# Kernel optimization log

Measured on AMD Instinct MI355X. Metric: run time of the kernel, lower is better.

The kernel has to match this reference:

```python
import jax, jax.numpy as jnp
import numpy as np

B, T, D = 4, 2048, 1024
H = 16
HD = D // H


def setup_inputs() -> dict:
    key = jax.random.key(0)
    ks = jax.random.split(key, 9)
    s = 1.0 / np.sqrt(D)
    return {
        "x": jax.random.normal(ks[0], (B, T, D), dtype=jnp.float32),
        "Wk": jax.random.normal(ks[1], (D, D), dtype=jnp.float32) * s,
        "bk": jnp.zeros((D,), dtype=jnp.float32),
        "Wq": jax.random.normal(ks[2], (D, D), dtype=jnp.float32) * s,
        "bq": jnp.zeros((D,), dtype=jnp.float32),
        "Wv": jax.random.normal(ks[3], (D, D), dtype=jnp.float32) * s,
        "bv": jnp.zeros((D,), dtype=jnp.float32),
        "Wp": jax.random.normal(ks[4], (D, D), dtype=jnp.float32) * s,
        "bp": jnp.zeros((D,), dtype=jnp.float32),
    }


def reference(x, Wk, bk, Wq, bq, Wv, bv, Wp, bp):
    Bv, Tv, Dv = x.shape
    # project and split heads: [B, H, T, HD]
    def heads(w, b):
        return (x @ w + b).reshape(Bv, Tv, H, HD).transpose(0, 2, 1, 3)
    k = heads(Wk, bk)
    q = heads(Wq, bq)
    v = heads(Wv, bv)
    scale = 1.0 / np.sqrt(HD)
    att = jnp.einsum('bhqd,bhkd->bhqk', q, k) * scale  # [B,H,T,T]
    causal = jnp.tril(jnp.ones((Tv, Tv), dtype=bool))
    att = jnp.where(causal[None, None, :, :], att, -jnp.inf)
    att = jax.nn.softmax(att, axis=-1)
    y = jnp.einsum('bhqk,bhkd->bhqd', att, v)  # [B,H,T,HD]
    y = y.transpose(0, 2, 1, 3).reshape(Bv, Tv, Dv)
    return y @ Wp + bp
```

## Files before the change

### kernel.cpp

```cpp
#include <hip/hip_runtime.h>
#include <stdint.h>

#define Bb 4
#define Tt 2048
#define Dd 1024
#define Hh 16
#define HDd 64
#define Mm 8192

typedef __attribute__((ext_vector_type(8))) short bf16x8;
typedef __attribute__((ext_vector_type(4))) float f32x4;
typedef __attribute__((ext_vector_type(16))) float f32x16;

#define MFMA(a, b, c) __builtin_amdgcn_mfma_f32_16x16x32_bf16(a, b, c, 0, 0, 0)
#define MFMA32(a, b, c) __builtin_amdgcn_mfma_f32_32x32x16_bf16(a, b, c, 0, 0, 0)

#define LOG2E 1.44269504088896340736f
#if __has_builtin(__builtin_amdgcn_exp2f)
#define EXP2(x) __builtin_amdgcn_exp2f(x)
#else
#define EXP2(x) __expf((x) * 0.69314718055994530942f)
#endif

union vfu { uint2 u2[2]; bf16x8 v; };
union apu { uint32_t u[4]; bf16x8 v; };

__device__ __forceinline__ unsigned short f2b(float f) {
  union { float f; uint32_t u; } v; v.f = f;
  return (unsigned short)((v.u + 0x7FFFu + ((v.u >> 16) & 1u)) >> 16);
}

__device__ __forceinline__ uint32_t pk2(float a, float b) {
  union { __bf16 h[2]; uint32_t u; } x;
  x.h[0] = (__bf16)a; x.h[1] = (__bf16)b;
  return x.u;
}

__device__ __forceinline__ void gload_lds16(const void* g, void* l) {
  __builtin_amdgcn_global_load_lds(
      (const __attribute__((address_space(1))) void*)g,
      (__attribute__((address_space(3))) void*)l, 16, 0, 0);
}

__global__ __launch_bounds__(256) void k_convert_x(const float* __restrict__ x,
                                                   unsigned short* __restrict__ xb) {
  int i = (blockIdx.x * 256 + threadIdx.x) * 8;
  float4 a = *(const float4*)(x + i);
  float4 b = *(const float4*)(x + i + 4);
  uint4 o;
  o.x = f2b(a.x) | ((uint32_t)f2b(a.y) << 16);
  o.y = f2b(a.z) | ((uint32_t)f2b(a.w) << 16);
  o.z = f2b(b.x) | ((uint32_t)f2b(b.y) << 16);
  o.w = f2b(b.z) | ((uint32_t)f2b(b.w) << 16);
  *(uint4*)(xb + i) = o;
}

__global__ __launch_bounds__(256) void k_transpose_w(
    const float* __restrict__ Wk, const float* __restrict__ Wq,
    const float* __restrict__ Wv, const float* __restrict__ Wp,
    unsigned short* __restrict__ WkT, unsigned short* __restrict__ WqT,
    unsigned short* __restrict__ WvT, unsigned short* __restrict__ WpT) {
  const float* W; unsigned short* O;
  int wsel = blockIdx.y;
  W = wsel == 0 ? Wk : wsel == 1 ? Wq : wsel == 2 ? Wv : Wp;
  O = wsel == 0 ? WkT : wsel == 1 ? WqT : wsel == 2 ? WvT : WpT;
  __shared__ unsigned short tile[32][36];
  int kb = (blockIdx.x >> 5) << 5;
  int nb = (blockIdx.x & 31) << 5;
  int t = threadIdx.x;
  int r = t >> 3, c4 = (t & 7) << 2;
  float4 v = *(const float4*)(W + (size_t)(kb + r) * Dd + nb + c4);
  tile[r][c4 + 0] = f2b(v.x); tile[r][c4 + 1] = f2b(v.y);
  tile[r][c4 + 2] = f2b(v.z); tile[r][c4 + 3] = f2b(v.w);
  __syncthreads();
  uint2 o;
  o.x = tile[c4 + 0][r] | ((uint32_t)tile[c4 + 1][r] << 16);
  o.y = tile[c4 + 2][r] | ((uint32_t)tile[c4 + 3][r] << 16);
  *(uint2*)(O + (size_t)(nb + r) * Dd + kb + c4) = o;
}

__global__ __launch_bounds__(256, 2) void k_gemm3(
    const unsigned short* __restrict__ A,
    const unsigned short* __restrict__ BtQ, const unsigned short* __restrict__ BtK,
    const unsigned short* __restrict__ BtV,
    const float* __restrict__ bq, const float* __restrict__ bk,
    const float* __restrict__ bv,
    unsigned short* __restrict__ Qb, unsigned short* __restrict__ Kb,
    unsigned short* __restrict__ VTb) {
  __shared__ __align__(16) unsigned short Al[2][128 * 32];
  __shared__ __align__(16) unsigned short Bl[2][3][128 * 32];
  int tid = threadIdx.x;
  int lane = tid & 63, wid = tid >> 6;
  int wr = wid >> 1, wc = wid & 1;
  int lq = lane & 15, lh = lane >> 4;
  int mb = blockIdx.x * 128;
  int nb = blockIdx.y << 7;

  int srow = (wid << 5) + (lane >> 2);
  int scol = (lane & 3) << 3;
  const unsigned short* Ag = A + (size_t)(mb + srow) * Dd + scol;
  const unsigned short* Bg0 = BtQ + (size_t)(nb + srow) * Dd + scol;
  const unsigned short* Bg1 = BtK + (size_t)(nb + srow) * Dd + scol;
  const unsigned short* Bg2 = BtV + (size_t)(nb + srow) * Dd + scol;
  int lofs = wid << 10;

#define STAGE3(kb_, bi_) do {                                            \
    gload_lds16(Ag + (kb_), &Al[bi_][0] + lofs);                         \
    gload_lds16(Ag + (kb_) + 16 * Dd, &Al[bi_][0] + lofs + 16 * 32);     \
    gload_lds16(Bg0 + (kb_), &Bl[bi_][0][0] + lofs);                     \
    gload_lds16(Bg0 + (kb_) + 16 * Dd, &Bl[bi_][0][0] + lofs + 16 * 32); \
    gload_lds16(Bg1 + (kb_), &Bl[bi_][1][0] + lofs);                     \
    gload_lds16(Bg1 + (kb_) + 16 * Dd, &Bl[bi_][1][0] + lofs + 16 * 32); \
    gload_lds16(Bg2 + (kb_), &Bl[bi_][2][0] + lofs);                     \
    gload_lds16(Bg2 + (kb_) + 16 * Dd, &Bl[bi_][2][0] + lofs + 16 * 32); \
  } while (0)

  f32x4 zero = {0.f, 0.f, 0.f, 0.f};
  f32x4 acc[3][4][4];
#pragma unroll
  for (int s = 0; s < 3; s++)
#pragma unroll
    for (int m = 0; m < 4; m++)
#pragma unroll
      for (int n = 0; n < 4; n++) acc[s][m][n] = zero;

  STAGE3(0, 0);
  __syncthreads();

  int cur = 0;
  for (int kb = 0; kb < Dd; kb += 32) {
    if (kb + 32 < Dd) STAGE3(kb + 32, cur ^ 1);
    bf16x8 af[4];
#pragma unroll
    for (int m = 0; m < 4; m++)
      af[m] = *(const bf16x8*)(&Al[cur][0] +
                               (((wr << 6) + (m << 4) + lq) << 5) + (lh << 3));
#pragma unroll
    for (int s = 0; s < 3; s++) {
      bf16x8 bf[4];
#pragma unroll
      for (int n = 0; n < 4; n++)
        bf[n] = *(const bf16x8*)(&Bl[cur][s][0] +
                                 (((wc << 6) + (n << 4) + lq) << 5) + (lh << 3));
      __builtin_amdgcn_s_setprio(1);
#pragma unroll
      for (int m = 0; m < 4; m++)
#pragma unroll
        for (int n = 0; n < 4; n++) acc[s][m][n] = MFMA(af[m], bf[n], acc[s][m][n]);
      __builtin_amdgcn_s_setprio(0);
    }
    __syncthreads();
    cur ^= 1;
  }
#undef STAGE3

  int b_idx = mb >> 11;
#pragma unroll
  for (int s = 0; s < 3; s++) {
#pragma unroll
    for (int n = 0; n < 4; n++) {
      int col = nb + (wc << 6) + (n << 4) + lq;
      float bbias = (s == 0) ? bq[col] : (s == 1) ? bk[col] : bv[col];
      int hh = col >> 6, hd = col & 63;
#pragma unroll
      for (int m = 0; m < 4; m++) {
        int row0 = mb + (wr << 6) + (m << 4) + (lh << 2);
        int t0 = row0 & 2047;
        if (s == 2) {
          float v0 = acc[s][m][n][0] + bbias, v1 = acc[s][m][n][1] + bbias;
          float v2 = acc[s][m][n][2] + bbias, v3 = acc[s][m][n][3] + bbias;
          uint2 pv;
          pv.x = f2b(v0) | ((uint32_t)f2b(v1) << 16);
          pv.y = f2b(v2) | ((uint32_t)f2b(v3) << 16);
          int t0s = t0 ^ ((hd & 7) << 3);
          *(uint2*)(VTb + ((size_t)(b_idx * 16 + hh) * 64 + hd) * Tt + t0s) = pv;
        } else {
          unsigned short* O = (s == 0) ? Qb : Kb;
          float sc = (s == 0) ? (0.125f * LOG2E) : 1.0f;
#pragma unroll
          for (int r = 0; r < 4; r++) {
            float v = (acc[s][m][n][r] + bbias) * sc;
            int trow = t0 + r;
            int hds = (s == 0) ? hd : (hd ^ ((trow & 7) << 3));
            O[((size_t)(b_idx * 16 + hh) * Tt + trow) * 64 + hds] = f2b(v);
          }
        }
      }
    }
  }
}

__global__ __launch_bounds__(256) void k_gemm(
    const unsigned short* __restrict__ A,
    const unsigned short* __restrict__ Bt0,
    const float* __restrict__ bias0,
    float* __restrict__ Pout) {
  __shared__ __align__(16) unsigned short Al[2][128 * 32];
  __shared__ __align__(16) unsigned short Bl[2][128 * 32];
  int tid = threadIdx.x;
  int lane = tid & 63, wid = tid >> 6;
  int wr = wid >> 1, wc = wid & 1;
  int lq = lane & 15, lh = lane >> 4;
  int mb = blockIdx.x * 128;
  int nb = blockIdx.y << 7;

  int srow = (wid << 5) + (lane >> 2);
  int scol = (lane & 3) << 3;
  const unsigned short* Ag = A + (size_t)(mb + srow) * Dd + scol;
  const unsigned short* Bg = Bt0 + (size_t)(nb + srow) * Dd + scol;
  int lofs = wid << 10;

#define STAGEP(kb_, bi_) do {                                            \
    gload_lds16(Ag + (kb_), &Al[bi_][0] + lofs);                         \
    gload_lds16(Ag + (kb_) + 16 * Dd, &Al[bi_][0] + lofs + 16 * 32);     \
    gload_lds16(Bg + (kb_), &Bl[bi_][0] + lofs);                         \
    gload_lds16(Bg + (kb_) + 16 * Dd, &Bl[bi_][0] + lofs + 16 * 32);     \
  } while (0)

  f32x4 zero = {0.f, 0.f, 0.f, 0.f};
  f32x4 acc[4][4];
#pragma unroll
  for (int m = 0; m < 4; m++)
#pragma unroll
    for (int n = 0; n < 4; n++) acc[m][n] = zero;

  STAGEP(0, 0);
  __syncthreads();

  int cur = 0;
  for (int kb = 0; kb < Dd; kb += 32) {
    if (kb + 32 < Dd) STAGEP(kb + 32, cur ^ 1);
    bf16x8 af[4], bf[4];
#pragma unroll
    for (int m = 0; m < 4; m++)
      af[m] = *(const bf16x8*)(&Al[cur][0] +
                               (((wr << 6) + (m << 4) + lq) << 5) + (lh << 3));
#pragma unroll
    for (int n = 0; n < 4; n++)
      bf[n] = *(const bf16x8*)(&Bl[cur][0] +
                               (((wc << 6) + (n << 4) + lq) << 5) + (lh << 3));
    __builtin_amdgcn_s_setprio(1);
#pragma unroll
    for (int m = 0; m < 4; m++)
#pragma unroll
      for (int n = 0; n < 4; n++) acc[m][n] = MFMA(af[m], bf[n], acc[m][n]);
    __builtin_amdgcn_s_setprio(0);
    __syncthreads();
    cur ^= 1;
  }
#undef STAGEP

#pragma unroll
  for (int n = 0; n < 4; n++) {
    int col = nb + (wc << 6) + (n << 4) + lq;
    float bb = bias0[col];
#pragma unroll
    for (int m = 0; m < 4; m++) {
      int row0 = mb + (wr << 6) + (m << 4) + (lh << 2);
#pragma unroll
      for (int r = 0; r < 4; r++)
        Pout[(size_t)(row0 + r) * Dd + col] = acc[m][n][r] + bb;
    }
  }
}

__global__ __launch_bounds__(256, 2) void k_attn(
    const unsigned short* __restrict__ Qb, const unsigned short* __restrict__ Kb,
    const unsigned short* __restrict__ VTb, unsigned short* __restrict__ yb) {
  __shared__ __align__(16) unsigned short KL[2][8192];
  __shared__ __align__(16) unsigned short VL[2][8192];
  int b = blockIdx.x;
  int p = b >> 6;
  int rr6 = b & 63;
  int bh = ((rr6 & 7) << 3) | (rr6 >> 3);
  int tid = threadIdx.x, lane = tid & 63, w = tid >> 6;
  int l31 = lane & 31, hi = lane >> 5;
  const unsigned short* __restrict__ Qh = Qb + (size_t)bh * Tt * 64;
  const unsigned short* __restrict__ Kh = Kb + (size_t)bh * Tt * 64;
  const unsigned short* __restrict__ Vh = VTb + (size_t)bh * 64 * Tt;
  int qgA = (p << 7) + (w << 5);
  int qgB = ((15 - p) << 7) + (w << 5);

  bf16x8 qfA[4], qfB[4];
#pragma unroll
  for (int c = 0; c < 4; c++) {
    qfA[c] = *(const bf16x8*)(Qh + (size_t)(qgA + l31) * 64 + (c << 4) + (hi << 3));
    qfB[c] = *(const bf16x8*)(Qh + (size_t)(qgB + l31) * 64 + (c << 4) + (hi << 3));
  }

  f32x16 accA0, accA1, accB0, accB1, accLA, accLB;
#pragma unroll
  for (int i = 0; i < 16; i++) {
    accA0[i] = 0.f; accA1[i] = 0.f; accB0[i] = 0.f; accB1[i] = 0.f;
    accLA[i] = 0.f; accLB[i] = 0.f;
  }
  apu onesf;
  onesf.u[0] = onesf.u[1] = onesf.u[2] = onesf.u[3] = 0x3F803F80u;

  int jmaxb = 15 - p;
  int srowK = lane >> 3, scolK = (lane & 7) << 3;
  int rowbK = w << 5;
  int srowV = lane >> 4, scolV = (lane & 15) << 3;
  int rowbV = w << 4;
  int swz = l31 & 7;

#define STAGE(kvt_, bi_) do {                                                        \
    int kv_ = (kvt_) << 7;                                                           \
    gload_lds16(Kh + (size_t)(kv_ + rowbK + srowK) * 64 + scolK,                     \
                &KL[bi_][rowbK << 6]);                                               \
    gload_lds16(Kh + (size_t)(kv_ + rowbK + 8 + srowK) * 64 + scolK,                 \
                &KL[bi_][(rowbK + 8) << 6]);                                         \
    gload_lds16(Kh + (size_t)(kv_ + rowbK + 16 + srowK) * 64 + scolK,                \
                &KL[bi_][(rowbK + 16) << 6]);                                        \
    gload_lds16(Kh + (size_t)(kv_ + rowbK + 24 + srowK) * 64 + scolK,                \
                &KL[bi_][(rowbK + 24) << 6]);                                        \
    gload_lds16(Vh + (size_t)(rowbV + srowV) * Tt + kv_ + scolV,                     \
                &VL[bi_][rowbV << 7]);                                               \
    gload_lds16(Vh + (size_t)(rowbV + 4 + srowV) * Tt + kv_ + scolV,                 \
                &VL[bi_][(rowbV + 4) << 7]);                                         \
    gload_lds16(Vh + (size_t)(rowbV + 8 + srowV) * Tt + kv_ + scolV,                 \
                &VL[bi_][(rowbV + 8) << 7]);                                         \
    gload_lds16(Vh + (size_t)(rowbV + 12 + srowV) * Tt + kv_ + scolV,                \
                &VL[bi_][(rowbV + 12) << 7]);                                        \
  } while (0)

  STAGE(0, 0);
  __syncthreads();

  int cur = 0;
  for (int jt = 0; jt <= jmaxb; ++jt) {
    if (jt < jmaxb) STAGE(jt + 1, cur ^ 1);
    int base_kv = jt << 7;
    const unsigned short* KB = &KL[cur][0];
    const unsigned short* VB = &VL[cur][0];
#pragma unroll
    for (int n2 = 0; n2 < 4; n2++) {
      int relB = qgB - base_kv - (n2 << 5);
      int relA = qgA - base_kv - (n2 << 5);
      if (relB >= 0) {
        bool doA = (relA >= 0);
        bf16x8 kf[4];
        int krowb = ((n2 << 5) + l31) << 6;
#pragma unroll
        for (int c = 0; c < 4; c++)
          kf[c] = *(const bf16x8*)(KB + krowb + ((((c << 1) + hi) ^ swz) << 3));
        f32x16 sA, sB;
#pragma unroll
        for (int i = 0; i < 16; i++) { sA[i] = 0.f; sB[i] = 0.f; }
        __builtin_amdgcn_s_setprio(1);
        if (doA) {
#pragma unroll
          for (int c = 0; c < 4; c++) {
            sA = MFMA32(kf[c], qfA[c], sA);
            sB = MFMA32(kf[c], qfB[c], sB);
          }
        } else {
#pragma unroll
          for (int c = 0; c < 4; c++) sB = MFMA32(kf[c], qfB[c], sB);
        }
        __builtin_amdgcn_s_setprio(0);
        float pA[16], pB[16];
        if (relB == 0) {
          int rB = l31;
#pragma unroll
          for (int r = 0; r < 16; r++) {
            int krow = (r & 3) + ((r >> 2) << 3) + (hi << 2);
            pB[r] = EXP2(krow > rB ? -1e30f : sB[r]);
          }
        } else {
#pragma unroll
          for (int r = 0; r < 16; r++) pB[r] = EXP2(sB[r]);
        }
        if (doA) {
          if (relA == 0) {
            int rA = l31;
#pragma unroll
            for (int r = 0; r < 16; r++) {
              int krow = (r & 3) + ((r >> 2) << 3) + (hi << 2);
              pA[r] = EXP2(krow > rA ? -1e30f : sA[r]);
            }
          } else {
#pragma unroll
            for (int r = 0; r < 16; r++) pA[r] = EXP2(sA[r]);
          }
        }
        vfu vf[2][2];
#pragma unroll
        for (int n2v = 0; n2v < 2; n2v++) {
          int vrowb = ((n2v << 5) + l31) << 7;
#pragma unroll
          for (int cc = 0; cc < 2; cc++) {
            int blk0 = (n2 << 2) + (cc << 1);
            vf[n2v][cc].u2[0] =
                *(const uint2*)(VB + vrowb + ((blk0 ^ swz) << 3) + (hi << 2));
            vf[n2v][cc].u2[1] =
                *(const uint2*)(VB + vrowb + (((blk0 + 1) ^ swz) << 3) + (hi << 2));
          }
        }
        apu b0, b1;
#pragma unroll
        for (int g = 0; g < 4; g++) {
          b0.u[g] = pk2(pB[2 * g], pB[2 * g + 1]);
          b1.u[g] = pk2(pB[8 + 2 * g], pB[8 + 2 * g + 1]);
        }
        __builtin_amdgcn_s_setprio(1);
        accB0 = MFMA32(b0.v, vf[0][0].v, accB0);
        accB1 = MFMA32(b0.v, vf[1][0].v, accB1);
        accLB = MFMA32(b0.v, onesf.v, accLB);
        accB0 = MFMA32(b1.v, vf[0][1].v, accB0);
        accB1 = MFMA32(b1.v, vf[1][1].v, accB1);
        accLB = MFMA32(b1.v, onesf.v, accLB);
        __builtin_amdgcn_s_setprio(0);
        if (doA) {
          apu a0, a1;
#pragma unroll
          for (int g = 0; g < 4; g++) {
            a0.u[g] = pk2(pA[2 * g], pA[2 * g + 1]);
            a1.u[g] = pk2(pA[8 + 2 * g], pA[8 + 2 * g + 1]);
          }
          __builtin_amdgcn_s_setprio(1);
          accA0 = MFMA32(a0.v, vf[0][0].v, accA0);
          accA1 = MFMA32(a0.v, vf[1][0].v, accA1);
          accLA = MFMA32(a0.v, onesf.v, accLA);
          accA0 = MFMA32(a1.v, vf[0][1].v, accA0);
          accA1 = MFMA32(a1.v, vf[1][1].v, accA1);
          accLA = MFMA32(a1.v, onesf.v, accLA);
          __builtin_amdgcn_s_setprio(0);
        }
      }
    }
    __syncthreads();
    cur ^= 1;
  }
#undef STAGE

  int bb = bh >> 4, hh = bh & 15;
#pragma unroll
  for (int r = 0; r < 16; r++) {
    int qr = (r & 3) + ((r >> 2) << 3) + (hi << 2);
    float invqA = 1.0f / accLA[r];
    float invqB = 1.0f / accLB[r];
    size_t baseA = ((size_t)(bb * Tt + qgA + qr)) * Dd + (hh << 6) + l31;
    size_t baseB = ((size_t)(bb * Tt + qgB + qr)) * Dd + (hh << 6) + l31;
    yb[baseA] = f2b(accA0[r] * invqA);
    yb[baseA + 32] = f2b(accA1[r] * invqA);
    yb[baseB] = f2b(accB0[r] * invqB);
    yb[baseB + 32] = f2b(accB1[r] * invqB);
  }
}

extern "C" void kernel_launch(void* const* d_in, const int* in_sizes, int n_in,
                              void* d_out, int out_size, void* d_ws, size_t ws_size,
                              hipStream_t stream) {
  const float* x = (const float*)d_in[0];
  const float* Wk = (const float*)d_in[1];
  const float* bk = (const float*)d_in[2];
  const float* Wq = (const float*)d_in[3];
  const float* bq = (const float*)d_in[4];
  const float* Wv = (const float*)d_in[5];
  const float* bv = (const float*)d_in[6];
  const float* Wp = (const float*)d_in[7];
  const float* bp = (const float*)d_in[8];
  float* out = (float*)d_out;

  char* ws = (char*)d_ws;
  unsigned short* xb  = (unsigned short*)(ws);
  unsigned short* WkT = (unsigned short*)(ws + (16ull << 20));
  unsigned short* WqT = (unsigned short*)(ws + (18ull << 20));
  unsigned short* WvT = (unsigned short*)(ws + (20ull << 20));
  unsigned short* WpT = (unsigned short*)(ws + (22ull << 20));
  unsigned short* Qb  = (unsigned short*)(ws + (24ull << 20));
  unsigned short* Kb  = (unsigned short*)(ws + (40ull << 20));
  unsigned short* VTb = (unsigned short*)(ws + (56ull << 20));
  unsigned short* yb  = (unsigned short*)(ws + (72ull << 20));

  k_convert_x<<<4096, 256, 0, stream>>>(x, xb);
  k_transpose_w<<<dim3(1024, 4), 256, 0, stream>>>(Wk, Wq, Wv, Wp, WkT, WqT, WvT, WpT);
  k_gemm3<<<dim3(64, 8), 256, 0, stream>>>(xb, WqT, WkT, WvT, bq, bk, bv,
                                           Qb, Kb, VTb);
  k_attn<<<512, 256, 0, stream>>>(Qb, Kb, VTb, yb);
  k_gemm<<<dim3(64, 8), 256, 0, stream>>>(yb, WpT, bp, out);
}
```

Before: 153.3 us.

## Merge conversion kernels and XOR-swizzle LDS tiles in projection GEMMs

```diff
diff --git a/kernel.cpp b/kernel.cpp
--- a/kernel.cpp
+++ b/kernel.cpp
@@ -42,41 +42,44 @@
       (__attribute__((address_space(3))) void*)l, 16, 0, 0);
 }
 
-__global__ __launch_bounds__(256) void k_convert_x(const float* __restrict__ x,
-                                                   unsigned short* __restrict__ xb) {
-  int i = (blockIdx.x * 256 + threadIdx.x) * 8;
-  float4 a = *(const float4*)(x + i);
-  float4 b = *(const float4*)(x + i + 4);
-  uint4 o;
-  o.x = f2b(a.x) | ((uint32_t)f2b(a.y) << 16);
-  o.y = f2b(a.z) | ((uint32_t)f2b(a.w) << 16);
-  o.z = f2b(b.x) | ((uint32_t)f2b(b.y) << 16);
-  o.w = f2b(b.z) | ((uint32_t)f2b(b.w) << 16);
-  *(uint4*)(xb + i) = o;
-}
-
-__global__ __launch_bounds__(256) void k_transpose_w(
+__global__ __launch_bounds__(256) void k_front(
+    const float* __restrict__ x, unsigned short* __restrict__ xb,
     const float* __restrict__ Wk, const float* __restrict__ Wq,
     const float* __restrict__ Wv, const float* __restrict__ Wp,
     unsigned short* __restrict__ WkT, unsigned short* __restrict__ WqT,
     unsigned short* __restrict__ WvT, unsigned short* __restrict__ WpT) {
-  const float* W; unsigned short* O;
-  int wsel = blockIdx.y;
-  W = wsel == 0 ? Wk : wsel == 1 ? Wq : wsel == 2 ? Wv : Wp;
-  O = wsel == 0 ? WkT : wsel == 1 ? WqT : wsel == 2 ? WvT : WpT;
   __shared__ unsigned short tile[32][36];
-  int kb = (blockIdx.x >> 5) << 5;
-  int nb = (blockIdx.x & 31) << 5;
-  int t = threadIdx.x;
-  int r = t >> 3, c4 = (t & 7) << 2;
-  float4 v = *(const float4*)(W + (size_t)(kb + r) * Dd + nb + c4);
-  tile[r][c4 + 0] = f2b(v.x); tile[r][c4 + 1] = f2b(v.y);
-  tile[r][c4 + 2] = f2b(v.z); tile[r][c4 + 3] = f2b(v.w);
-  __syncthreads();
-  uint2 o;
-  o.x = tile[c4 + 0][r] | ((uint32_t)tile[c4 + 1][r] << 16);
-  o.y = tile[c4 + 2][r] | ((uint32_t)tile[c4 + 3][r] << 16);
-  *(uint2*)(O + (size_t)(nb + r) * Dd + kb + c4) = o;
+  int b = blockIdx.x;
+  if (b < 4096) {
+    int i = (b * 256 + threadIdx.x) * 8;
+    float4 a = *(const float4*)(x + i);
+    float4 c = *(const float4*)(x + i + 4);
+    uint4 o;
+    o.x = f2b(a.x) | ((uint32_t)f2b(a.y) << 16);
+    o.y = f2b(a.z) | ((uint32_t)f2b(a.w) << 16);
+    o.z = f2b(c.x) | ((uint32_t)f2b(c.y) << 16);
+    o.w = f2b(c.z) | ((uint32_t)f2b(c.w) << 16);
+    *(uint4*)(xb + i) = o;
+  } else {
+    int bb = b - 4096;
+    int wsel = bb >> 10;
+    int bx = bb & 1023;
+    const float* W; unsigned short* O;
+    W = wsel == 0 ? Wk : wsel == 1 ? Wq : wsel == 2 ? Wv : Wp;
+    O = wsel == 0 ? WkT : wsel == 1 ? WqT : wsel == 2 ? WvT : WpT;
+    int kb = (bx >> 5) << 5;
+    int nb = (bx & 31) << 5;
+    int t = threadIdx.x;
+    int r = t >> 3, c4 = (t & 7) << 2;
+    float4 v = *(const float4*)(W + (size_t)(kb + r) * Dd + nb + c4);
+    tile[r][c4 + 0] = f2b(v.x); tile[r][c4 + 1] = f2b(v.y);
+    tile[r][c4 + 2] = f2b(v.z); tile[r][c4 + 3] = f2b(v.w);
+    __syncthreads();
+    uint2 o;
+    o.x = tile[c4 + 0][r] | ((uint32_t)tile[c4 + 1][r] << 16);
+    o.y = tile[c4 + 2][r] | ((uint32_t)tile[c4 + 3][r] << 16);
+    *(uint2*)(O + (size_t)(nb + r) * Dd + kb + c4) = o;
+  }
 }
 
 __global__ __launch_bounds__(256, 2) void k_gemm3(
@@ -97,12 +100,13 @@
   int nb = blockIdx.y << 7;
 
   int srow = (wid << 5) + (lane >> 2);
-  int scol = (lane & 3) << 3;
+  int scol = (((lane & 3) ^ ((lane >> 2) & 3)) << 3);
   const unsigned short* Ag = A + (size_t)(mb + srow) * Dd + scol;
   const unsigned short* Bg0 = BtQ + (size_t)(nb + srow) * Dd + scol;
   const unsigned short* Bg1 = BtK + (size_t)(nb + srow) * Dd + scol;
   const unsigned short* Bg2 = BtV + (size_t)(nb + srow) * Dd + scol;
   int lofs = wid << 10;
+  int rsw = (lh ^ (lq & 3)) << 3;
 
 #define STAGE3(kb_, bi_) do {                                            \
     gload_lds16(Ag + (kb_), &Al[bi_][0] + lofs);                         \
@@ -134,14 +138,14 @@
 #pragma unroll
     for (int m = 0; m < 4; m++)
       af[m] = *(const bf16x8*)(&Al[cur][0] +
-                               (((wr << 6) + (m << 4) + lq) << 5) + (lh << 3));
+                               (((wr << 6) + (m << 4) + lq) << 5) + rsw);
 #pragma unroll
     for (int s = 0; s < 3; s++) {
       bf16x8 bf[4];
 #pragma unroll
       for (int n = 0; n < 4; n++)
         bf[n] = *(const bf16x8*)(&Bl[cur][s][0] +
-                                 (((wc << 6) + (n << 4) + lq) << 5) + (lh << 3));
+                                 (((wc << 6) + (n << 4) + lq) << 5) + rsw);
       __builtin_amdgcn_s_setprio(1);
 #pragma unroll
       for (int m = 0; m < 4; m++)
@@ -205,10 +209,11 @@
   int nb = blockIdx.y << 7;
 
   int srow = (wid << 5) + (lane >> 2);
-  int scol = (lane & 3) << 3;
+  int scol = (((lane & 3) ^ ((lane >> 2) & 3)) << 3);
   const unsigned short* Ag = A + (size_t)(mb + srow) * Dd + scol;
   const unsigned short* Bg = Bt0 + (size_t)(nb + srow) * Dd + scol;
   int lofs = wid << 10;
+  int rsw = (lh ^ (lq & 3)) << 3;
 
 #define STAGEP(kb_, bi_) do {                                            \
     gload_lds16(Ag + (kb_), &Al[bi_][0] + lofs);                         \
@@ -234,11 +239,11 @@
 #pragma unroll
     for (int m = 0; m < 4; m++)
       af[m] = *(const bf16x8*)(&Al[cur][0] +
-                               (((wr << 6) + (m << 4) + lq) << 5) + (lh << 3));
+                               (((wr << 6) + (m << 4) + lq) << 5) + rsw);
 #pragma unroll
     for (int n = 0; n < 4; n++)
       bf[n] = *(const bf16x8*)(&Bl[cur][0] +
-                               (((wc << 6) + (n << 4) + lq) << 5) + (lh << 3));
+                               (((wc << 6) + (n << 4) + lq) << 5) + rsw);
     __builtin_amdgcn_s_setprio(1);
 #pragma unroll
     for (int m = 0; m < 4; m++)
@@ -474,8 +479,7 @@
   unsigned short* VTb = (unsigned short*)(ws + (56ull << 20));
   unsigned short* yb  = (unsigned short*)(ws + (72ull << 20));
 
-  k_convert_x<<<4096, 256, 0, stream>>>(x, xb);
-  k_transpose_w<<<dim3(1024, 4), 256, 0, stream>>>(Wk, Wq, Wv, Wp, WkT, WqT, WvT, WpT);
+  k_front<<<8192, 256, 0, stream>>>(x, xb, Wk, Wq, Wv, Wp, WkT, WqT, WvT, WpT);
   k_gemm3<<<dim3(64, 8), 256, 0, stream>>>(xb, WqT, WkT, WvT, bq, bk, bv,
                                            Qb, Kb, VTb);
   k_attn<<<512, 256, 0, stream>>>(Qb, Kb, VTb, yb);
```

Result: no change. 151.6 us (-1.1%).
